# Performance work log

Measured on AMD Instinct MI355X. Metric: run time of the kernel, lower is better.

The kernel has to match this reference:

```python
import jax, jax.numpy as jnp
import numpy as np

N, E, G = 40000, 640000, 64
D_IN, D_EMB, D_HID, D_OUT = 128, 128, 128, 36


def setup_inputs() -> dict:
    key = jax.random.key(0)
    ks = jax.random.split(key, 12)
    x = jax.random.normal(ks[0], (N, D_IN), dtype=jnp.float32)
    edge_weight = jax.random.uniform(ks[1], (E,), dtype=jnp.float32)
    rho = jax.random.uniform(ks[2], (G,), dtype=jnp.float32)
    edge_index = jax.random.randint(ks[3], (2, E), 0, N, dtype=jnp.int32)
    batch = jnp.sort(jax.random.randint(ks[4], (N,), 0, G, dtype=jnp.int32))
    def lin(k, fi, fo):
        s = 1.0 / np.sqrt(fi)
        return jax.random.normal(k, (fi, fo), dtype=jnp.float32) * s
    conv_w = lin(ks[5], D_IN, D_EMB)
    conv_b = jnp.zeros((D_EMB,), jnp.float32)
    w1 = lin(ks[6], 2 * D_EMB + 1, D_HID); b1 = jnp.zeros((D_HID,), jnp.float32)
    w2 = lin(ks[7], D_HID, D_HID);        b2 = jnp.zeros((D_HID,), jnp.float32)
    w3 = lin(ks[8], D_HID, D_OUT);        b3 = jnp.zeros((D_OUT,), jnp.float32)
    return dict(x=x, edge_weight=edge_weight, rho=rho, conv_w=conv_w, conv_b=conv_b,
                w1=w1, b1=b1, w2=w2, b2=b2, w3=w3, b3=b3,
                edge_index=edge_index, batch=batch)


def _gcn_conv(h, edge_index, ew, W, b):
    # PyG GCNConv: add self-loops (weight 1), symmetric deg^-1/2 normalization,
    # linear transform, gather-scale-scatter aggregation, bias.
    n = h.shape[0]
    loop = jnp.arange(n, dtype=edge_index.dtype)
    src = jnp.concatenate([edge_index[0], loop])
    dst = jnp.concatenate([edge_index[1], loop])
    w_all = jnp.concatenate([ew, jnp.ones((n,), ew.dtype)])
    deg = jax.ops.segment_sum(w_all, dst, num_segments=n)
    dinv = jnp.where(deg > 0, jax.lax.rsqrt(deg), 0.0)
    norm = dinv[src] * w_all * dinv[dst]          # [E+N]
    hW = h @ W                                    # [N, D_EMB]
    msg = hW[src] * norm[:, None]                 # [E+N, D_EMB]
    return jax.ops.segment_sum(msg, dst, num_segments=n) + b


def reference(x, edge_weight, rho, conv_w, conv_b, w1, b1, w2, b2, w3, b3,
              edge_index, batch):
    h = jax.nn.relu(_gcn_conv(x, edge_index, edge_weight, conv_w, conv_b))
    g = G
    cnt = jax.ops.segment_sum(jnp.ones((h.shape[0],), h.dtype), batch, num_segments=g)
    hmax = jax.ops.segment_max(h, batch, num_segments=g)
    hmax = jnp.where(cnt[:, None] > 0, hmax, 0.0)
    hsum = jax.ops.segment_sum(h, batch, num_segments=g)
    hmean = hsum / jnp.maximum(cnt, 1.0)[:, None]
    hg = jnp.concatenate([hmax, hmean, rho[:, None]], axis=1)  # [G, 2*D_EMB+1]
    z = jax.nn.relu(hg @ w1 + b1)
    z = jax.nn.relu(z @ w2 + b2)
    return z @ w3 + b3
```

## Files before the change

kernel.cpp:

```cpp
#include <hip/hip_runtime.h>
#include <hip/hip_bf16.h>
#include <hip/hip_fp16.h>

static __device__ __forceinline__ float relu_f(float v) { return v > 0.f ? v : 0.f; }

typedef _Float16 half8 __attribute__((ext_vector_type(8)));
typedef float floatx4 __attribute__((ext_vector_type(4)));


__global__ void cast_init_kernel(const float4* __restrict__ x4, __half2* __restrict__ xh2,
                                 int n4, int* __restrict__ indeg, int n,
                                 float* __restrict__ gmax, float* __restrict__ gsum,
                                 float* __restrict__ gcnt, int gch, int g,
                                 const float* __restrict__ W, _Float16* __restrict__ wt,
                                 int2* __restrict__ epack, int epad) {
  int i = blockIdx.x * blockDim.x + threadIdx.x;
  if (i < n4) {
    float4 v = x4[i];
    xh2[2 * i + 0] = __floats2half2_rn(v.x, v.y);
    xh2[2 * i + 1] = __floats2half2_rn(v.z, v.w);
  }
  if (i < n) indeg[i] = 0;
  if (i < gch) { gmax[i] = 0.f; gsum[i] = 0.f; }
  if (i < g) gcnt[i] = 0.f;
  if (i < 128 * 128) {
    int k = i >> 7, nn = i & 127;
    wt[nn * 128 + k] = (_Float16)W[i];
  }
  if (i < epad) epack[i] = make_int2(0, 0);
}

__global__ void count_rank_kernel(const int* __restrict__ dst, int* __restrict__ indeg,
                                  int* __restrict__ rank, int E) {
  int e = blockIdx.x * blockDim.x + threadIdx.x;
  if (e >= E) return;
  rank[e] = atomicAdd(&indeg[dst[e]], 1);
}


__global__ __launch_bounds__(1024) void scan_reduce_kernel(const int* __restrict__ indeg,
                                                           int* __restrict__ bsum, int n) {
  int i = blockIdx.x * 1024 + threadIdx.x;
  int v = (i < n) ? ((indeg[i] + 3) & ~3) : 0;
  #pragma unroll
  for (int off = 32; off; off >>= 1) v += __shfl_down(v, off, 64);
  __shared__ int ws[16];
  int lane = threadIdx.x & 63, wid = threadIdx.x >> 6;
  if (lane == 0) ws[wid] = v;
  __syncthreads();
  if (threadIdx.x == 0) {
    int s = 0;
    #pragma unroll
    for (int j = 0; j < 16; ++j) s += ws[j];
    bsum[blockIdx.x] = s;
  }
}

__global__ __launch_bounds__(1024) void scan_write_kernel(const int* __restrict__ indeg,
    const int* __restrict__ bsum, int* __restrict__ rowptr, int n, int nb) {
  int i = blockIdx.x * 1024 + threadIdx.x;
  int v = (i < n) ? ((indeg[i] + 3) & ~3) : 0;
  int lane = threadIdx.x & 63, wid = threadIdx.x >> 6;
  int inc = v;
  #pragma unroll
  for (int off = 1; off < 64; off <<= 1) {
    int u = __shfl_up(inc, off, 64);
    if (lane >= off) inc += u;
  }
  __shared__ int wtot[16];
  __shared__ int s_off;
  if (lane == 63) wtot[wid] = inc;
  if (threadIdx.x < 64) {
    int acc = 0;
    for (int base = 0; base < nb; base += 64) {
      int idx = base + (int)threadIdx.x;
      int val = (idx < nb && idx < (int)blockIdx.x) ? bsum[idx] : 0;
      #pragma unroll
      for (int off = 32; off; off >>= 1) val += __shfl_down(val, off, 64);
      if (threadIdx.x == 0) acc += val;
    }
    if (threadIdx.x == 0) s_off = acc;
  }
  __syncthreads();
  int woff = 0;
  for (int j = 0; j < wid; ++j) woff += wtot[j];
  int excl = s_off + woff + inc - v;
  if (i < n) {
    rowptr[i + 1] = excl + v;
    if (i == 0) rowptr[0] = 0;
  }
}

__global__ void edge_fill_kernel(const int* __restrict__ src, const int* __restrict__ dst,
                                 const float* __restrict__ ew, const int* __restrict__ rank,
                                 const int* __restrict__ rowptr, int2* __restrict__ epack,
                                 int E) {
  int e = blockIdx.x * blockDim.x + threadIdx.x;
  if (e >= E) return;
  int d = dst[e];
  int slot = rowptr[d] + rank[e];
  epack[slot] = make_int2(src[e], __float_as_int(ew[e]));
}

__global__ void row_dinv_kernel(const int* __restrict__ rowptr, const int2* __restrict__ epack,
                                float* __restrict__ dinv, int n) {
  int i = blockIdx.x * blockDim.x + threadIdx.x;
  if (i >= n) return;
  int s = rowptr[i], e = rowptr[i + 1];
  float d = 1.0f;
  for (int j = s; j < e; ++j) d += __int_as_float(epack[j].y);
  dinv[i] = (d > 0.f) ? rsqrtf(d) : 0.f;
}


__global__ __launch_bounds__(256) void aggregate_kernel(const half8* __restrict__ xh8,
    const float* __restrict__ dinv, const int* __restrict__ rowptr,
    const int2* __restrict__ epack, half8* __restrict__ aggh8, int n) {
  int gid = blockIdx.x * blockDim.x + threadIdx.x;
  int lane = gid & 63;
  int grp = lane >> 4, sub = lane & 15;
  int node = (gid >> 6) * 4 + grp;
  if (node >= n) return;
  float dn = dinv[node];
  half8 xv = xh8[(size_t)node * 16 + sub];
  float sw = dn * dn;
  float acc[8];
  #pragma unroll
  for (int c = 0; c < 8; ++c) acc[c] = sw * (float)xv[c];
  int s = rowptr[node], e = rowptr[node + 1];
  for (int j = s; j < e; j += 4) {
    int2 pk0 = epack[j + 0];
    int2 pk1 = epack[j + 1];
    int2 pk2 = epack[j + 2];
    int2 pk3 = epack[j + 3];
    half8 h0 = xh8[(size_t)pk0.x * 16 + sub];
    half8 h1 = xh8[(size_t)pk1.x * 16 + sub];
    half8 h2 = xh8[(size_t)pk2.x * 16 + sub];
    half8 h3 = xh8[(size_t)pk3.x * 16 + sub];
    float w0 = dinv[pk0.x] * __int_as_float(pk0.y) * dn;
    float w1 = dinv[pk1.x] * __int_as_float(pk1.y) * dn;
    float w2 = dinv[pk2.x] * __int_as_float(pk2.y) * dn;
    float w3 = dinv[pk3.x] * __int_as_float(pk3.y) * dn;
    #pragma unroll
    for (int c = 0; c < 8; ++c) {
      acc[c] += w0 * (float)h0[c];
      acc[c] += w1 * (float)h1[c];
      acc[c] += w2 * (float)h2[c];
      acc[c] += w3 * (float)h3[c];
    }
  }
  half8 outv;
  #pragma unroll
  for (int c = 0; c < 8; ++c) outv[c] = (_Float16)acc[c];
  aggh8[(size_t)node * 16 + sub] = outv;
}


__global__ __launch_bounds__(256) void gemm_pool_kernel(const _Float16* __restrict__ aggh,
    const _Float16* __restrict__ wt, const float* __restrict__ bias,
    const int* __restrict__ batch, float* __restrict__ gmax, float* __restrict__ gsum,
    float* __restrict__ gcnt, int n) {
  __shared__ float sH[64 * 129];
  __shared__ int sBatch[64];
  int tid = threadIdx.x;
  int w = tid >> 6, lane = tid & 63;
  int quad = lane >> 4, c15 = lane & 15;
  int row0 = blockIdx.x * 64;
  int nb = n - row0; if (nb > 64) nb = 64;

  float bb[8];
  #pragma unroll
  for (int j = 0; j < 8; ++j) bb[j] = bias[j * 16 + c15];

  int arow = row0 + w * 16 + c15;
  if (arow >= n) arow = n - 1;
  const half8* aptr = (const half8*)(aggh + (size_t)arow * 128 + quad * 8);

  floatx4 acc[8] = {};
  #pragma unroll
  for (int ks = 0; ks < 4; ++ks) {
    half8 af = aptr[ks * 4];
    #pragma unroll
    for (int j = 0; j < 8; ++j) {
      const half8* bptr =
          (const half8*)(wt + (size_t)(j * 16 + c15) * 128 + ks * 32 + quad * 8);
      acc[j] = __builtin_amdgcn_mfma_f32_16x16x32_f16(af, *bptr, acc[j], 0, 0, 0);
    }
  }

  if (tid < nb) sBatch[tid] = batch[row0 + tid];

  #pragma unroll
  for (int j = 0; j < 8; ++j) {
    int col = j * 16 + c15;
    #pragma unroll
    for (int r = 0; r < 4; ++r) {
      int row = w * 16 + quad * 4 + r;
      if (row < nb) sH[row * 129 + col] = relu_f(acc[j][r] + bb[j]);
    }
  }
  __syncthreads();

  int c = tid & 127, hf = tid >> 7;
  int r0 = hf * 32, r1 = r0 + 32;
  if (r1 > nb) r1 = nb;
  if (r0 < r1) {
    int cur = sBatch[r0];
    float mx = 0.f, sm = 0.f;
    int cnt = 0;
    for (int r = r0; r < r1; ++r) {
      int g = sBatch[r];
      if (g != cur) {
        atomicMax((int*)&gmax[cur * 128 + c], __float_as_int(mx));
        atomicAdd(&gsum[cur * 128 + c], sm);
        if (c == 0) atomicAdd(&gcnt[cur], (float)cnt);
        mx = 0.f; sm = 0.f; cnt = 0; cur = g;
      }
      float v = sH[r * 129 + c];
      mx = fmaxf(mx, v);
      sm += v;
      ++cnt;
    }
    atomicMax((int*)&gmax[cur * 128 + c], __float_as_int(mx));
    atomicAdd(&gsum[cur * 128 + c], sm);
    if (c == 0) atomicAdd(&gcnt[cur], (float)cnt);
  }
}


__global__ __launch_bounds__(128) void mlp_kernel(const float* __restrict__ gmax,
    const float* __restrict__ gsum, const float* __restrict__ gcnt,
    const float* __restrict__ rho,
    const float* __restrict__ w1, const float* __restrict__ b1,
    const float* __restrict__ w2, const float* __restrict__ b2,
    const float* __restrict__ w3, const float* __restrict__ b3,
    float* __restrict__ out) {
  __shared__ float s_in[257];
  __shared__ float s_z1[128];
  __shared__ float s_z2[128];
  int g = blockIdx.x, t = threadIdx.x;
  float inv_cnt = 1.f / fmaxf(gcnt[g], 1.f);
  s_in[t] = gmax[g * 128 + t];
  s_in[128 + t] = gsum[g * 128 + t] * inv_cnt;
  if (t == 0) s_in[256] = rho[g];
  __syncthreads();
  float s = b1[t];
  for (int k = 0; k < 257; ++k) s += s_in[k] * w1[k * 128 + t];
  s_z1[t] = relu_f(s);
  __syncthreads();
  s = b2[t];
  for (int k = 0; k < 128; ++k) s += s_z1[k] * w2[k * 128 + t];
  s_z2[t] = relu_f(s);
  __syncthreads();
  if (t < 36) {
    s = b3[t];
    for (int k = 0; k < 128; ++k) s += s_z2[k] * w3[k * 36 + t];
    out[g * 36 + t] = s;
  }
}


extern "C" void kernel_launch(void* const* d_in, const int* in_sizes, int n_in,
                              void* d_out, int out_size, void* d_ws, size_t ws_size,
                              hipStream_t stream) {
  const float* x      = (const float*)d_in[0];
  const float* ew     = (const float*)d_in[1];
  const float* rho    = (const float*)d_in[2];
  const float* conv_w = (const float*)d_in[3];
  const float* conv_b = (const float*)d_in[4];
  const float* w1 = (const float*)d_in[5];
  const float* b1 = (const float*)d_in[6];
  const float* w2 = (const float*)d_in[7];
  const float* b2 = (const float*)d_in[8];
  const float* w3 = (const float*)d_in[9];
  const float* b3 = (const float*)d_in[10];
  const int* eidx  = (const int*)d_in[11];
  const int* batch = (const int*)d_in[12];

  const int N = in_sizes[0] / 128;
  const int E = in_sizes[1];
  const int G = in_sizes[2];
  const int* srcp = eidx;
  const int* dstp = eidx + E;

  const int NB = (N + 1023) / 1024;
  const int EPAD = E + 4 * N;

  char* p = (char*)d_ws;
  auto carve = [&](size_t bytes) { char* r = p; p += (bytes + 255) & ~(size_t)255; return (void*)r; };
  float*    dinv   = (float*)   carve((size_t)N * 4);
  int*      indeg  = (int*)     carve((size_t)N * 4);
  int*      rowptr = (int*)     carve((size_t)(N + 1) * 4);
  int*      rank   = (int*)     carve((size_t)E * 4);
  int*      bsum   = (int*)     carve((size_t)NB * 4);
  int2*     epack  = (int2*)    carve((size_t)EPAD * 8);
  __half2*  xh     = (__half2*) carve((size_t)N * 128 * 2);
  _Float16* aggh   = (_Float16*)carve((size_t)N * 128 * 2);
  _Float16* wt     = (_Float16*)carve((size_t)128 * 128 * 2);
  float*    gmax   = (float*)   carve((size_t)G * 128 * 4);
  float*    gsum   = (float*)   carve((size_t)G * 128 * 4);
  float*    gcnt   = (float*)   carve((size_t)G * 4);

  const int n4 = N * 32;

  cast_init_kernel<<<(n4 + 255) / 256, 256, 0, stream>>>((const float4*)x, xh, n4,
                                                         indeg, N, gmax, gsum, gcnt,
                                                         G * 128, G, conv_w, wt,
                                                         epack, EPAD);
  count_rank_kernel<<<(E + 255) / 256, 256, 0, stream>>>(dstp, indeg, rank, E);
  scan_reduce_kernel<<<NB, 1024, 0, stream>>>(indeg, bsum, N);
  scan_write_kernel<<<NB, 1024, 0, stream>>>(indeg, bsum, rowptr, N, NB);
  edge_fill_kernel<<<(E + 255) / 256, 256, 0, stream>>>(srcp, dstp, ew, rank, rowptr, epack, E);
  row_dinv_kernel<<<(N + 255) / 256, 256, 0, stream>>>(rowptr, epack, dinv, N);
  aggregate_kernel<<<(N + 15) / 16, 256, 0, stream>>>((const half8*)xh, dinv, rowptr, epack,
                                                      (half8*)aggh, N);
  gemm_pool_kernel<<<(N + 63) / 64, 256, 0, stream>>>(aggh, wt, conv_b, batch,
                                                      gmax, gsum, gcnt, N);
  mlp_kernel<<<G, 128, 0, stream>>>(gmax, gsum, gcnt, rho, w1, b1, w2, b2, w3, b3,
                                    (float*)d_out);
}
```

Baseline: 215.6 us.

## Fuse CSR build preprocessing into one cooperative kernel with grid syncs

Replaces the six preprocessing launches (cast/init, count/rank, the two scan passes, edge fill, dinv) with a single cooperative kernel of 512 blocks that separates phases with grid.sync(). Each thread keeps the dst, src, weight and atomic rank of up to 8 edges in registers between phases, so the global rank array is no longer written and re-read. The block-level scan now runs over 512 blocks of 256 threads and writes per-block sums before a grid barrier. The aim is to cut per-launch overhead and intermediate memory traffic, in exchange for several grid-wide barriers and a fixed grid that covers at most 8 edges per thread, which limits the edge count it can handle.

```diff
diff --git a/kernel.cpp b/kernel.cpp
--- a/kernel.cpp
+++ b/kernel.cpp
@@ -1,115 +1,115 @@
 #include <hip/hip_runtime.h>
 #include <hip/hip_bf16.h>
 #include <hip/hip_fp16.h>
+#include <hip/hip_cooperative_groups.h>
+
+namespace cg = cooperative_groups;
 
 static __device__ __forceinline__ float relu_f(float v) { return v > 0.f ? v : 0.f; }
 
 typedef _Float16 half8 __attribute__((ext_vector_type(8)));
 typedef float floatx4 __attribute__((ext_vector_type(4)));
 
-
-__global__ void cast_init_kernel(const float4* __restrict__ x4, __half2* __restrict__ xh2,
-                                 int n4, int* __restrict__ indeg, int n,
-                                 float* __restrict__ gmax, float* __restrict__ gsum,
-                                 float* __restrict__ gcnt, int gch, int g,
-                                 const float* __restrict__ W, _Float16* __restrict__ wt,
-                                 int2* __restrict__ epack, int epad) {
-  int i = blockIdx.x * blockDim.x + threadIdx.x;
-  if (i < n4) {
+#define MEGA_BLOCKS 512
+#define MEGA_THREADS 256
+#define MEGA_NT (MEGA_BLOCKS * MEGA_THREADS)
+
+
+__global__ __launch_bounds__(MEGA_THREADS) void build_kernel(
+    const float4* __restrict__ x4, __half2* __restrict__ xh2, int n4,
+    const float* __restrict__ W, _Float16* __restrict__ wt,
+    const int* __restrict__ src, const int* __restrict__ dst,
+    const float* __restrict__ ew,
+    int* __restrict__ indeg, int* __restrict__ bsum, int* __restrict__ rowptr,
+    int2* __restrict__ epack, float* __restrict__ dinv,
+    float* __restrict__ gmax, float* __restrict__ gsum, float* __restrict__ gcnt,
+    int N, int E, int EPAD, int G) {
+  cg::grid_group grid = cg::this_grid();
+  int tid = blockIdx.x * MEGA_THREADS + threadIdx.x;
+
+  for (int i = tid; i < n4; i += MEGA_NT) {
     float4 v = x4[i];
     xh2[2 * i + 0] = __floats2half2_rn(v.x, v.y);
     xh2[2 * i + 1] = __floats2half2_rn(v.z, v.w);
   }
-  if (i < n) indeg[i] = 0;
-  if (i < gch) { gmax[i] = 0.f; gsum[i] = 0.f; }
-  if (i < g) gcnt[i] = 0.f;
-  if (i < 128 * 128) {
+  for (int i = tid; i < EPAD; i += MEGA_NT) epack[i] = make_int2(0, 0);
+  for (int i = tid; i < N; i += MEGA_NT) indeg[i] = 0;
+  for (int i = tid; i < G * 128; i += MEGA_NT) { gmax[i] = 0.f; gsum[i] = 0.f; }
+  for (int i = tid; i < G; i += MEGA_NT) gcnt[i] = 0.f;
+  for (int i = tid; i < 128 * 128; i += MEGA_NT) {
     int k = i >> 7, nn = i & 127;
     wt[nn * 128 + k] = (_Float16)W[i];
   }
-  if (i < epad) epack[i] = make_int2(0, 0);
-}
-
-__global__ void count_rank_kernel(const int* __restrict__ dst, int* __restrict__ indeg,
-                                  int* __restrict__ rank, int E) {
-  int e = blockIdx.x * blockDim.x + threadIdx.x;
-  if (e >= E) return;
-  rank[e] = atomicAdd(&indeg[dst[e]], 1);
-}
-
-
-__global__ __launch_bounds__(1024) void scan_reduce_kernel(const int* __restrict__ indeg,
-                                                           int* __restrict__ bsum, int n) {
-  int i = blockIdx.x * 1024 + threadIdx.x;
-  int v = (i < n) ? ((indeg[i] + 3) & ~3) : 0;
-  #pragma unroll
-  for (int off = 32; off; off >>= 1) v += __shfl_down(v, off, 64);
-  __shared__ int ws[16];
-  int lane = threadIdx.x & 63, wid = threadIdx.x >> 6;
-  if (lane == 0) ws[wid] = v;
-  __syncthreads();
-  if (threadIdx.x == 0) {
-    int s = 0;
+  grid.sync();
+
+  int rd[8], rr[8], rs[8], rw[8];
+  #pragma unroll
+  for (int k = 0; k < 8; ++k) {
+    int e = tid + k * MEGA_NT;
+    if (e < E) {
+      int d = dst[e];
+      rd[k] = d;
+      rs[k] = src[e];
+      rw[k] = __float_as_int(ew[e]);
+      rr[k] = atomicAdd(&indeg[d], 1);
+    }
+  }
+  grid.sync();
+
+  {
+    int i = tid;
+    int v = (i < N) ? ((indeg[i] + 3) & ~3) : 0;
+    int lane = threadIdx.x & 63, wid = threadIdx.x >> 6;
+    int inc = v;
     #pragma unroll
-    for (int j = 0; j < 16; ++j) s += ws[j];
-    bsum[blockIdx.x] = s;
-  }
-}
-
-__global__ __launch_bounds__(1024) void scan_write_kernel(const int* __restrict__ indeg,
-    const int* __restrict__ bsum, int* __restrict__ rowptr, int n, int nb) {
-  int i = blockIdx.x * 1024 + threadIdx.x;
-  int v = (i < n) ? ((indeg[i] + 3) & ~3) : 0;
-  int lane = threadIdx.x & 63, wid = threadIdx.x >> 6;
-  int inc = v;
-  #pragma unroll
-  for (int off = 1; off < 64; off <<= 1) {
-    int u = __shfl_up(inc, off, 64);
-    if (lane >= off) inc += u;
-  }
-  __shared__ int wtot[16];
-  __shared__ int s_off;
-  if (lane == 63) wtot[wid] = inc;
-  if (threadIdx.x < 64) {
-    int acc = 0;
-    for (int base = 0; base < nb; base += 64) {
-      int idx = base + (int)threadIdx.x;
-      int val = (idx < nb && idx < (int)blockIdx.x) ? bsum[idx] : 0;
-      #pragma unroll
-      for (int off = 32; off; off >>= 1) val += __shfl_down(val, off, 64);
-      if (threadIdx.x == 0) acc += val;
-    }
-    if (threadIdx.x == 0) s_off = acc;
-  }
-  __syncthreads();
-  int woff = 0;
-  for (int j = 0; j < wid; ++j) woff += wtot[j];
-  int excl = s_off + woff + inc - v;
-  if (i < n) {
-    rowptr[i + 1] = excl + v;
-    if (i == 0) rowptr[0] = 0;
-  }
-}
-
-__global__ void edge_fill_kernel(const int* __restrict__ src, const int* __restrict__ dst,
-                                 const float* __restrict__ ew, const int* __restrict__ rank,
-                                 const int* __restrict__ rowptr, int2* __restrict__ epack,
-                                 int E) {
-  int e = blockIdx.x * blockDim.x + threadIdx.x;
-  if (e >= E) return;
-  int d = dst[e];
-  int slot = rowptr[d] + rank[e];
-  epack[slot] = make_int2(src[e], __float_as_int(ew[e]));
-}
-
-__global__ void row_dinv_kernel(const int* __restrict__ rowptr, const int2* __restrict__ epack,
-                                float* __restrict__ dinv, int n) {
-  int i = blockIdx.x * blockDim.x + threadIdx.x;
-  if (i >= n) return;
-  int s = rowptr[i], e = rowptr[i + 1];
-  float d = 1.0f;
-  for (int j = s; j < e; ++j) d += __int_as_float(epack[j].y);
-  dinv[i] = (d > 0.f) ? rsqrtf(d) : 0.f;
+    for (int off = 1; off < 64; off <<= 1) {
+      int u = __shfl_up(inc, off, 64);
+      if (lane >= off) inc += u;
+    }
+    __shared__ int wtot[4];
+    __shared__ int s_off;
+    if (lane == 63) wtot[wid] = inc;
+    __syncthreads();
+    if (threadIdx.x == 0) bsum[blockIdx.x] = wtot[0] + wtot[1] + wtot[2] + wtot[3];
+    grid.sync();
+    if (threadIdx.x < 64) {
+      int acc = 0;
+      for (int base = 0; base < MEGA_BLOCKS; base += 64) {
+        int idx = base + (int)threadIdx.x;
+        int val = (idx < (int)blockIdx.x) ? bsum[idx] : 0;
+        #pragma unroll
+        for (int off = 32; off; off >>= 1) val += __shfl_down(val, off, 64);
+        if (threadIdx.x == 0) acc += val;
+      }
+      if (threadIdx.x == 0) s_off = acc;
+    }
+    __syncthreads();
+    int woff = 0;
+    for (int j = 0; j < wid; ++j) woff += wtot[j];
+    int excl = s_off + woff + inc - v;
+    if (i < N) {
+      rowptr[i + 1] = excl + v;
+      if (i == 0) rowptr[0] = 0;
+    }
+  }
+  grid.sync();
+
+  #pragma unroll
+  for (int k = 0; k < 8; ++k) {
+    int e = tid + k * MEGA_NT;
+    if (e < E) {
+      int slot = rowptr[rd[k]] + rr[k];
+      epack[slot] = make_int2(rs[k], rw[k]);
+    }
+  }
+  grid.sync();
+
+  for (int i = tid; i < N; i += MEGA_NT) {
+    int s = rowptr[i], e2 = rowptr[i + 1];
+    float d = 1.0f;
+    for (int j = s; j < e2; ++j) d += __int_as_float(epack[j].y);
+    dinv[i] = (d > 0.f) ? rsqrtf(d) : 0.f;
+  }
 }
 
 
@@ -283,7 +283,6 @@
   const int* srcp = eidx;
   const int* dstp = eidx + E;
 
-  const int NB = (N + 1023) / 1024;
   const int EPAD = E + 4 * N;
 
   char* p = (char*)d_ws;
@@ -291,8 +290,7 @@
   float*    dinv   = (float*)   carve((size_t)N * 4);
   int*      indeg  = (int*)     carve((size_t)N * 4);
   int*      rowptr = (int*)     carve((size_t)(N + 1) * 4);
-  int*      rank   = (int*)     carve((size_t)E * 4);
-  int*      bsum   = (int*)     carve((size_t)NB * 4);
+  int*      bsum   = (int*)     carve((size_t)MEGA_BLOCKS * 4);
   int2*     epack  = (int2*)    carve((size_t)EPAD * 8);
   __half2*  xh     = (__half2*) carve((size_t)N * 128 * 2);
   _Float16* aggh   = (_Float16*)carve((size_t)N * 128 * 2);
@@ -301,17 +299,22 @@
   float*    gsum   = (float*)   carve((size_t)G * 128 * 4);
   float*    gcnt   = (float*)   carve((size_t)G * 4);
 
-  const int n4 = N * 32;
-
-  cast_init_kernel<<<(n4 + 255) / 256, 256, 0, stream>>>((const float4*)x, xh, n4,
-                                                         indeg, N, gmax, gsum, gcnt,
-                                                         G * 128, G, conv_w, wt,
-                                                         epack, EPAD);
-  count_rank_kernel<<<(E + 255) / 256, 256, 0, stream>>>(dstp, indeg, rank, E);
-  scan_reduce_kernel<<<NB, 1024, 0, stream>>>(indeg, bsum, N);
-  scan_write_kernel<<<NB, 1024, 0, stream>>>(indeg, bsum, rowptr, N, NB);
-  edge_fill_kernel<<<(E + 255) / 256, 256, 0, stream>>>(srcp, dstp, ew, rank, rowptr, epack, E);
-  row_dinv_kernel<<<(N + 255) / 256, 256, 0, stream>>>(rowptr, epack, dinv, N);
+  int n4 = N * 32;
+
+  const float4* x4p = (const float4*)x;
+  __half2* xhp = xh;
+  void* args[] = {
+    (void*)&x4p, (void*)&xhp, (void*)&n4,
+    (void*)&conv_w, (void*)&wt,
+    (void*)&srcp, (void*)&dstp, (void*)&ew,
+    (void*)&indeg, (void*)&bsum, (void*)&rowptr,
+    (void*)&epack, (void*)&dinv,
+    (void*)&gmax, (void*)&gsum, (void*)&gcnt,
+    (void*)&N, (void*)&E, (void*)&EPAD, (void*)&G
+  };
+  hipLaunchCooperativeKernel((void*)build_kernel, dim3(MEGA_BLOCKS), dim3(MEGA_THREADS),
+                             args, 0, stream);
+
   aggregate_kernel<<<(N + 15) / 16, 256, 0, stream>>>((const half8*)xh, dinv, rowptr, epack,
                                                       (half8*)aggh, N);
   gemm_pool_kernel<<<(N + 63) / 64, 256, 0, stream>>>(aggh, wt, conv_b, batch,
```

Result: slower. 519.8 us (+141.1%).
